# Performance work log

Hardware: AMD Instinct MI355X
Metric: run time of the kernel (lower is better)

## Reference

```python
import jax, jax.numpy as jnp
import numpy as np

N = 50000      # nodes
E = 800000     # edges (avg degree 16)
DIN = 500      # input_dim
HID = 100      # hid_dim (fixed in module)
DOUT = 64      # output_dim
EPS = 1e-5     # LayerNorm eps (torch default)


def _layer_norm(x, g, b):
    mu = jnp.mean(x, axis=-1, keepdims=True)
    var = jnp.var(x, axis=-1, keepdims=True)
    return (x - mu) / jnp.sqrt(var + EPS) * g + b


def _gcn_conv(x, src, tgt, W, b):
    # PyG GCNConv: self-loops + symmetric normalization + linear + scatter-add
    h = x @ W  # [N, out]
    idx = jnp.arange(N)
    src_sl = jnp.concatenate([src, idx])
    tgt_sl = jnp.concatenate([tgt, idx])
    deg = jax.ops.segment_sum(jnp.ones(src_sl.shape, h.dtype), tgt_sl, num_segments=N)
    dinv = jnp.where(deg > 0, deg ** -0.5, 0.0)
    norm = dinv[src_sl] * dinv[tgt_sl]  # [E+N]
    out = jax.ops.segment_sum(h[src_sl] * norm[:, None], tgt_sl, num_segments=N)
    return out + b


def setup_inputs() -> dict:
    key = jax.random.key(0)
    ks = jax.random.split(key, 10)
    glorot = lambda k, fi, fo: jax.random.normal(k, (fi, fo), jnp.float32) * np.float32(1.0 / np.sqrt(fi))
    z = lambda d: jnp.zeros((d,), jnp.float32)
    return dict(
        data_x=jax.random.normal(ks[0], (N, DIN), jnp.float32),
        data_edge_index=jax.random.randint(ks[1], (2, E), 0, N),
        data_edge_attr=jnp.zeros((E,), jnp.int32),  # single relation type
        t_W1=glorot(ks[2], DIN, HID), t_b1=z(HID), t_g1=jnp.ones((HID,), jnp.float32), t_be1=z(HID),
        t_W2=glorot(ks[3], HID, HID), t_b2=z(HID), t_g2=jnp.ones((HID,), jnp.float32), t_be2=z(HID),
        r_Wrel=glorot(ks[4], HID, HID)[None],  # [n_relations=1, H, H]
        r_Wself=glorot(ks[5], HID, HID), r_b=z(HID),
        c1_W=glorot(ks[6], HID, HID), c1_b=z(HID),
        c2_W=glorot(ks[7], HID, DOUT), c2_b=z(DOUT),
    )


def reference(data_x, data_edge_index, data_edge_attr,
              t_W1, t_b1, t_g1, t_be1, t_W2, t_b2, t_g2, t_be2,
              r_Wrel, r_Wself, r_b, c1_W, c1_b, c2_W, c2_b):
    src, tgt = data_edge_index[0], data_edge_index[1]
    # transform: Linear -> LN -> ReLU -> Linear -> LN -> ReLU
    x = jax.nn.relu(_layer_norm(data_x @ t_W1 + t_b1, t_g1, t_be1))
    x = jax.nn.relu(_layer_norm(x @ t_W2 + t_b2, t_g2, t_be2))
    # RGCN, n_relations=1, n_layers=1: per-relation message + self transform
    msgs = x[src] @ r_Wrel[0]  # edge_attr is all relation 0
    x = x @ r_Wself + jax.ops.segment_sum(msgs, tgt, num_segments=N) + r_b
    x = jax.nn.relu(x)  # dropout = identity (eval)
    x = jax.nn.relu(_gcn_conv(x, src, tgt, c1_W, c1_b))
    x = _gcn_conv(x, src, tgt, c2_W, c2_b)
    return jax.nn.log_softmax(x, axis=1)
```

## Files before the change

kernel.cpp:

```cpp
#include <hip/hip_runtime.h>
#include <hip/hip_bf16.h>

typedef __attribute__((ext_vector_type(8))) short short8;
typedef __attribute__((ext_vector_type(8))) unsigned short ushort8;
typedef __attribute__((ext_vector_type(4))) float f32x4;

static constexpr int NN = 50000;
static constexpr int NE = 800000;
static constexpr int SCAN_B = 196;

#define MFMA16x16x32 __builtin_amdgcn_mfma_f32_16x16x32_bf16

__device__ __forceinline__ float b2f(unsigned short u){
  unsigned v = ((unsigned)u) << 16;
  return __builtin_bit_cast(float, v);
}
__device__ __forceinline__ unsigned short f2b(float f){
  unsigned x = __builtin_bit_cast(unsigned, f);
  unsigned r = (x + 0x7fffu + ((x >> 16) & 1u)) >> 16;
  return (unsigned short)r;
}

__device__ __align__(256) int   g_isf32;
__device__ __align__(256) unsigned short g_W1t  [112 * 512];
__device__ __align__(256) unsigned short g_W2t  [112 * 128];
__device__ __align__(256) unsigned short g_WselfT[112 * 128];
__device__ __align__(256) unsigned short g_WrelT [112 * 128];
__device__ __align__(256) unsigned short g_c1Wt [112 * 128];
__device__ __align__(256) unsigned short g_c2Wt [64 * 128];
__device__ __align__(256) unsigned short g_bufA[(size_t)NN * 128];
__device__ __align__(256) unsigned short g_bufB[(size_t)NN * 128];
__device__ __align__(256) unsigned short g_bufC[(size_t)NN * 128];
__device__ __align__(256) int   g_deg[NN];
__device__ __align__(256) int   g_rowptr[NN + 1];
__device__ __align__(256) int   g_cursor[NN];
__device__ __align__(256) int   g_colidx[NE];
__device__ __align__(256) float g_dinv[NN];
__device__ __align__(256) int   g_partial[256];

__device__ __forceinline__ float ld_in(const void* p, int idx, int isf32){
  if (isf32) return ((const float*)p)[idx];
  return b2f(((const unsigned short*)p)[idx]);
}

__global__ void k_detect(const unsigned short* __restrict__ x){
  __shared__ int sh[256];
  int tid = threadIdx.x;
  int cnt = 0;
  for (int j = 0; j < 16; j++){
    unsigned short h = x[(size_t)(tid * 16 + j) * 2];
    int e = (h >> 7) & 0xFF;
    if (e >= 90 && e <= 160) cnt++;
  }
  sh[tid] = cnt;
  __syncthreads();
  for (int off = 128; off > 0; off >>= 1){
    if (tid < off) sh[tid] += sh[tid + off];
    __syncthreads();
  }
  if (tid == 0) g_isf32 = (sh[0] < 2458) ? 1 : 0;
}

__global__ void k_zero(){
  int i = blockIdx.x * 256 + threadIdx.x;
  if (i < NN){ g_deg[i] = 0; g_cursor[i] = 0; }
}

__device__ __forceinline__ void xp_one(const void* W, unsigned short* Wt, int idx,
                                       int K, int Nc, int Kpad, int isf32){
  int n = idx / Kpad;
  int k = idx - n * Kpad;
  float v = 0.f;
  if (n < Nc && k < K) v = ld_in(W, k * Nc + n, isf32);
  Wt[idx] = f2b(v);
}
__global__ void k_transpose_all(const void* W1, const void* W2, const void* Wself,
                                const void* Wrel, const void* c1W, const void* c2W){
  int idx = blockIdx.x * 256 + threadIdx.x;
  const int isf32 = g_isf32;
  if (idx < 57344){ xp_one(W1, g_W1t, idx, 500, 100, 512, isf32); return; }
  idx -= 57344;
  if (idx < 14336){ xp_one(W2,    g_W2t,    idx, 100, 100, 128, isf32); return; }
  idx -= 14336;
  if (idx < 14336){ xp_one(Wself, g_WselfT, idx, 100, 100, 128, isf32); return; }
  idx -= 14336;
  if (idx < 14336){ xp_one(Wrel,  g_WrelT,  idx, 100, 100, 128, isf32); return; }
  idx -= 14336;
  if (idx < 14336){ xp_one(c1W,   g_c1Wt,   idx, 100, 100, 128, isf32); return; }
  idx -= 14336;
  if (idx < 8192){  xp_one(c2W,   g_c2Wt,   idx, 100, 64,  128, isf32); }
}

__global__ void k_deg(const int* __restrict__ tgt){
  int e = blockIdx.x * 256 + threadIdx.x;
  if (e < NE) atomicAdd(&g_deg[tgt[e]], 1);
}

__global__ __launch_bounds__(256) void k_scan1(){
  __shared__ int sh[256];
  int t = threadIdx.x;
  int i = blockIdx.x * 256 + t;
  int val = (i < NN) ? g_deg[i] : 0;
  sh[t] = val;
  __syncthreads();
#pragma unroll
  for (int off = 1; off < 256; off <<= 1){
    int v = (t >= off) ? sh[t - off] : 0;
    __syncthreads();
    sh[t] += v;
    __syncthreads();
  }
  if (i < NN){
    g_rowptr[i] = sh[t] - val;
    g_dinv[i] = rsqrtf((float)(val + 1));
  }
  if (t == 255) g_partial[blockIdx.x] = sh[255];
}
__global__ __launch_bounds__(256) void k_scan2(){
  __shared__ int sh[256];
  int t = threadIdx.x;
  int val = (t < SCAN_B) ? g_partial[t] : 0;
  sh[t] = val;
  __syncthreads();
#pragma unroll
  for (int off = 1; off < 256; off <<= 1){
    int v = (t >= off) ? sh[t - off] : 0;
    __syncthreads();
    sh[t] += v;
    __syncthreads();
  }
  if (t < SCAN_B) g_partial[t] = sh[t] - val;
  if (t == 255) g_rowptr[NN] = sh[255];
}
__global__ __launch_bounds__(256) void k_scan3(){
  int i = blockIdx.x * 256 + threadIdx.x;
  if (i < NN) g_rowptr[i] += g_partial[blockIdx.x];
}

__global__ void k_fill(const int* __restrict__ src, const int* __restrict__ tgt){
  int e = blockIdx.x * 256 + threadIdx.x;
  if (e >= NE) return;
  int t = tgt[e];
  int pos = g_rowptr[t] + atomicAdd(&g_cursor[t], 1);
  g_colidx[pos] = src[e];
}

template<int MODE>
__global__ __launch_bounds__(256) void k_agg(){
  const unsigned short* x = (MODE == 1) ? g_bufC : g_bufB;
  int node = blockIdx.x * 16 + (threadIdx.x >> 4);
  if (node >= NN) return;
  const int c8 = (threadIdx.x & 15) * 8;

  float wt = (MODE != 0) ? g_dinv[node] : 1.f;
  float a[4][8];
#pragma unroll
  for (int j = 0; j < 4; j++)
#pragma unroll
    for (int k = 0; k < 8; k++) a[j][k] = 0.f;

  int p0 = g_rowptr[node], p1 = g_rowptr[node + 1];
  for (int p = p0; p < p1; p += 4){
    int   sj[4]; float wj[4];
#pragma unroll
    for (int j = 0; j < 4; j++){
      bool ok = (p + j) < p1;
      sj[j] = ok ? g_colidx[p + j] : node;
      wj[j] = ok ? ((MODE != 0) ? g_dinv[sj[j]] * wt : 1.f) : 0.f;
    }
    ushort8 r[4];
#pragma unroll
    for (int j = 0; j < 4; j++)
      r[j] = *reinterpret_cast<const ushort8*>(&x[(size_t)sj[j] * 128 + c8]);
#pragma unroll
    for (int j = 0; j < 4; j++)
#pragma unroll
      for (int k = 0; k < 8; k++) a[j][k] += wj[j] * b2f((unsigned short)r[j][k]);
  }
  if (MODE != 0){
    float ws = wt * wt;
    ushort8 sv = *reinterpret_cast<const ushort8*>(&x[(size_t)node * 128 + c8]);
#pragma unroll
    for (int k = 0; k < 8; k++) a[0][k] += ws * b2f((unsigned short)sv[k]);
  }
  ushort8 o;
#pragma unroll
  for (int k = 0; k < 8; k++)
    o[k] = f2b(a[0][k] + a[1][k] + a[2][k] + a[3][k]);
  *reinterpret_cast<ushort8*>(&g_bufA[(size_t)node * 128 + c8]) = o;
}

__global__ __launch_bounds__(256) void k_gemm1_ln(const void* __restrict__ Aext,
    const void* __restrict__ bias, const void* __restrict__ gamma,
    const void* __restrict__ beta){
  __shared__ unsigned short sA[64 * 136];
  const int tid = threadIdx.x;
  const int wave = tid >> 6, lane = tid & 63;
  const int m = lane & 15, q = lane >> 4;
  const int rowblk = blockIdx.x * 64;
  const int isf32 = g_isf32;
  const int srow = tid >> 5;
  const int scol = (tid & 31) * 4;
  f32x4 acc[7] = {};

  for (int kc = 0; kc < 4; kc++){
    __syncthreads();
#pragma unroll
    for (int ps = 0; ps < 8; ps++){
      int r = ps * 8 + srow;
      int grow = rowblk + r;
      int gcol = kc * 128 + scol;
      ushort4 vb = {0, 0, 0, 0};
      if (grow < NN && gcol + 4 <= 500){
        if (isf32){
          f32x4 v = *reinterpret_cast<const f32x4*>((const float*)Aext + (size_t)grow * 500 + gcol);
          vb.x = f2b(v[0]); vb.y = f2b(v[1]); vb.z = f2b(v[2]); vb.w = f2b(v[3]);
        } else {
          vb = *reinterpret_cast<const ushort4*>((const unsigned short*)Aext + (size_t)grow * 500 + gcol);
        }
      }
      *reinterpret_cast<ushort4*>(&sA[r * 136 + scol]) = vb;
    }
    __syncthreads();
#pragma unroll
    for (int c = 0; c < 4; c++){
      int k0 = c * 32 + q * 8;
      short8 a = *reinterpret_cast<const short8*>(&sA[(wave * 16 + m) * 136 + k0]);
      int gk0 = kc * 128 + k0;
#pragma unroll
      for (int t = 0; t < 7; t++){
        short8 b = *reinterpret_cast<const short8*>(g_W1t + (size_t)(t * 16 + m) * 512 + gk0);
        acc[t] = MFMA16x16x32(a, b, acc[t], 0, 0, 0);
      }
    }
  }

  float bf_[7], gf_[7], ef_[7];
#pragma unroll
  for (int t = 0; t < 7; t++){
    int col = t * 16 + m;
    bool ok = col < 100;
    bf_[t] = ok ? ld_in(bias, col, isf32)  : 0.f;
    gf_[t] = ok ? ld_in(gamma, col, isf32) : 0.f;
    ef_[t] = ok ? ld_in(beta, col, isf32)  : 0.f;
  }
  const int row0 = rowblk + wave * 16;
#pragma unroll
  for (int r = 0; r < 4; r++){
    float vals[7], s1 = 0.f, s2 = 0.f;
#pragma unroll
    for (int t = 0; t < 7; t++){
      int col = t * 16 + m;
      float v = (col < 100) ? (acc[t][r] + bf_[t]) : 0.f;
      vals[t] = v; s1 += v; s2 += v * v;
    }
#pragma unroll
    for (int msk = 1; msk < 16; msk <<= 1){
      s1 += __shfl_xor(s1, msk, 64);
      s2 += __shfl_xor(s2, msk, 64);
    }
    float mu = s1 * 0.01f;
    float var = fmaxf(s2 * 0.01f - mu * mu, 0.f);
    float rstd = rsqrtf(var + 1e-5f);
    int row = row0 + q * 4 + r;
    if (row < NN){
      unsigned short* orow = g_bufA + (size_t)row * 128;
#pragma unroll
      for (int t = 0; t < 7; t++){
        int col = t * 16 + m;
        float y = fmaxf((vals[t] - mu) * rstd * gf_[t] + ef_[t], 0.f);
        orow[col] = f2b((col < 100) ? y : 0.f);
      }
      orow[112 + m] = 0;
    }
  }
}

__global__ __launch_bounds__(256) void k_gemm2_ln(const void* __restrict__ bias,
    const void* __restrict__ gamma, const void* __restrict__ beta){
  const int isf32 = g_isf32;
  const int wave = threadIdx.x >> 6, lane = threadIdx.x & 63;
  const int m = lane & 15, q = lane >> 4;
  const int row0 = (blockIdx.x * 4 + wave) * 16;
  if (row0 >= NN) return;
  f32x4 acc[7] = {};
  const unsigned short* arow = g_bufA + (size_t)(row0 + m) * 128;
#pragma unroll
  for (int c = 0; c < 4; c++){
    const int k0 = c * 32 + q * 8;
    short8 a = *reinterpret_cast<const short8*>(arow + k0);
#pragma unroll
    for (int t = 0; t < 7; t++){
      short8 b = *reinterpret_cast<const short8*>(g_W2t + (size_t)(t * 16 + m) * 128 + k0);
      acc[t] = MFMA16x16x32(a, b, acc[t], 0, 0, 0);
    }
  }
  float bf_[7], gf_[7], ef_[7];
#pragma unroll
  for (int t = 0; t < 7; t++){
    int col = t * 16 + m;
    bool ok = col < 100;
    bf_[t] = ok ? ld_in(bias, col, isf32)  : 0.f;
    gf_[t] = ok ? ld_in(gamma, col, isf32) : 0.f;
    ef_[t] = ok ? ld_in(beta, col, isf32)  : 0.f;
  }
#pragma unroll
  for (int r = 0; r < 4; r++){
    float vals[7], s1 = 0.f, s2 = 0.f;
#pragma unroll
    for (int t = 0; t < 7; t++){
      int col = t * 16 + m;
      float v = (col < 100) ? (acc[t][r] + bf_[t]) : 0.f;
      vals[t] = v; s1 += v; s2 += v * v;
    }
#pragma unroll
    for (int msk = 1; msk < 16; msk <<= 1){
      s1 += __shfl_xor(s1, msk, 64);
      s2 += __shfl_xor(s2, msk, 64);
    }
    float mu = s1 * 0.01f;
    float var = fmaxf(s2 * 0.01f - mu * mu, 0.f);
    float rstd = rsqrtf(var + 1e-5f);
    unsigned short* orow = g_bufB + (size_t)(row0 + q * 4 + r) * 128;
#pragma unroll
    for (int t = 0; t < 7; t++){
      int col = t * 16 + m;
      float y = fmaxf((vals[t] - mu) * rstd * gf_[t] + ef_[t], 0.f);
      orow[col] = f2b((col < 100) ? y : 0.f);
    }
    orow[112 + m] = 0;
  }
}

template<int SEL>
__global__ __launch_bounds__(256) void k_gemm_bias_relu(const void* __restrict__ bias){
  const unsigned short* A1  = (SEL == 0) ? g_bufB : g_bufA;
  const unsigned short* B1t = (SEL == 0) ? g_WselfT : g_c1Wt;
  unsigned short* out       = (SEL == 0) ? g_bufC : g_bufB;
  const int isf32 = g_isf32;

  const int wave = threadIdx.x >> 6, lane = threadIdx.x & 63;
  const int m = lane & 15, q = lane >> 4;
  const int row0 = (blockIdx.x * 4 + wave) * 16;
  if (row0 >= NN) return;
  f32x4 acc[7] = {};
  const unsigned short* a1row = A1 + (size_t)(row0 + m) * 128;
#pragma unroll
  for (int c = 0; c < 4; c++){
    const int k0 = c * 32 + q * 8;
    short8 a = *reinterpret_cast<const short8*>(a1row + k0);
#pragma unroll
    for (int t = 0; t < 7; t++){
      short8 b = *reinterpret_cast<const short8*>(B1t + (size_t)(t * 16 + m) * 128 + k0);
      acc[t] = MFMA16x16x32(a, b, acc[t], 0, 0, 0);
    }
  }
  if (SEL == 0){
    const unsigned short* a2row = g_bufA + (size_t)(row0 + m) * 128;
#pragma unroll
    for (int c = 0; c < 4; c++){
      const int k0 = c * 32 + q * 8;
      short8 a = *reinterpret_cast<const short8*>(a2row + k0);
#pragma unroll
      for (int t = 0; t < 7; t++){
        short8 b = *reinterpret_cast<const short8*>(g_WrelT + (size_t)(t * 16 + m) * 128 + k0);
        acc[t] = MFMA16x16x32(a, b, acc[t], 0, 0, 0);
      }
    }
  }
  float bf_[7];
#pragma unroll
  for (int t = 0; t < 7; t++){
    int col = t * 16 + m;
    bf_[t] = (col < 100) ? ld_in(bias, col, isf32) : 0.f;
  }
#pragma unroll
  for (int r = 0; r < 4; r++){
    unsigned short* orow = out + (size_t)(row0 + q * 4 + r) * 128;
#pragma unroll
    for (int t = 0; t < 7; t++){
      int col = t * 16 + m;
      float y = fmaxf(acc[t][r] + bf_[t], 0.f);
      orow[col] = f2b((col < 100) ? y : 0.f);
    }
    orow[112 + m] = 0;
  }
}

__global__ __launch_bounds__(256) void k_gemm_lsm(const void* __restrict__ bias,
                                                  void* __restrict__ outv){
  const int isf32 = g_isf32;
  const int wave = threadIdx.x >> 6, lane = threadIdx.x & 63;
  const int m = lane & 15, q = lane >> 4;
  const int row0 = (blockIdx.x * 4 + wave) * 16;
  if (row0 >= NN) return;
  f32x4 acc[4] = {};
  const unsigned short* arow = g_bufA + (size_t)(row0 + m) * 128;
#pragma unroll
  for (int c = 0; c < 4; c++){
    const int k0 = c * 32 + q * 8;
    short8 a = *reinterpret_cast<const short8*>(arow + k0);
#pragma unroll
    for (int t = 0; t < 4; t++){
      short8 b = *reinterpret_cast<const short8*>(g_c2Wt + (size_t)(t * 16 + m) * 128 + k0);
      acc[t] = MFMA16x16x32(a, b, acc[t], 0, 0, 0);
    }
  }
  float bf_[4];
#pragma unroll
  for (int t = 0; t < 4; t++) bf_[t] = ld_in(bias, t * 16 + m, isf32);
#pragma unroll
  for (int r = 0; r < 4; r++){
    float vals[4], mx = -1e30f;
#pragma unroll
    for (int t = 0; t < 4; t++){
      float v = acc[t][r] + bf_[t];
      vals[t] = v; mx = fmaxf(mx, v);
    }
#pragma unroll
    for (int msk = 1; msk < 16; msk <<= 1) mx = fmaxf(mx, __shfl_xor(mx, msk, 64));
    float se = 0.f;
#pragma unroll
    for (int t = 0; t < 4; t++) se += expf(vals[t] - mx);
#pragma unroll
    for (int msk = 1; msk < 16; msk <<= 1) se += __shfl_xor(se, msk, 64);
    float lse = logf(se);
    size_t ro = (size_t)(row0 + q * 4 + r) * 64;
    if (isf32){
      float* orow = (float*)outv + ro;
#pragma unroll
      for (int t = 0; t < 4; t++) orow[t * 16 + m] = vals[t] - mx - lse;
    } else {
      unsigned short* orow = (unsigned short*)outv + ro;
#pragma unroll
      for (int t = 0; t < 4; t++) orow[t * 16 + m] = f2b(vals[t] - mx - lse);
    }
  }
}

extern "C" void kernel_launch(void* const* d_in, const int* in_sizes, int n_in,
                              void* d_out, int out_size, void* d_ws, size_t ws_size,
                              hipStream_t stream){
  (void)in_sizes; (void)n_in; (void)out_size; (void)d_ws; (void)ws_size;
  const void* data_x = d_in[0];
  const int* ei = (const int*)d_in[1];
  const int* src = ei;
  const int* tgt = ei + NE;
  const void *W1 = d_in[3], *b1 = d_in[4], *gm1 = d_in[5], *be1 = d_in[6];
  const void *W2 = d_in[7], *b2 = d_in[8], *gm2 = d_in[9], *be2 = d_in[10];
  const void *Wrel = d_in[11], *Wself = d_in[12], *rb = d_in[13];
  const void *c1W = d_in[14], *c1b = d_in[15];
  const void *c2W = d_in[16], *c2b = d_in[17];

  k_detect<<<1, 256, 0, stream>>>((const unsigned short*)data_x);
  k_zero<<<(NN + 255) / 256, 256, 0, stream>>>();
  k_transpose_all<<<(122880 + 255) / 256, 256, 0, stream>>>(W1, W2, Wself, Wrel, c1W, c2W);

  k_deg<<<(NE + 255) / 256, 256, 0, stream>>>(tgt);
  k_scan1<<<SCAN_B, 256, 0, stream>>>();
  k_scan2<<<1, 256, 0, stream>>>();
  k_scan3<<<SCAN_B, 256, 0, stream>>>();
  k_fill<<<(NE + 255) / 256, 256, 0, stream>>>(src, tgt);

  const int G64 = (NN + 63) / 64;
  const int GA  = (NN + 15) / 16;
  k_gemm1_ln<<<G64, 256, 0, stream>>>(data_x, b1, gm1, be1);
  k_gemm2_ln<<<G64, 256, 0, stream>>>(b2, gm2, be2);
  k_agg<0><<<GA, 256, 0, stream>>>();
  k_gemm_bias_relu<0><<<G64, 256, 0, stream>>>(rb);
  k_agg<1><<<GA, 256, 0, stream>>>();
  k_gemm_bias_relu<1><<<G64, 256, 0, stream>>>(c1b);
  k_agg<2><<<GA, 256, 0, stream>>>();
  k_gemm_lsm<<<G64, 256, 0, stream>>>(c2b, d_out);
}
```

Before: 526.1 us.

## Stream gemm1 A operand directly from global with register prefetch, one wave per block

The first GEMM+LayerNorm kernel stops staging the 500-wide input tile through shared memory with block-wide barriers. Each 64-thread block now handles 16 rows, and each lane loads its own row fragment straight from global memory, prefetching the next K-chunk into registers before the current MFMAs run. Out-of-range K columns are clamped to column 496; this is only correct if the padded rows of the transposed weight are zero. The change removes LDS traffic and __syncthreads stalls, at the cost of less coalesced per-instruction global access and smaller blocks.

```diff
diff --git a/kernel.cpp b/kernel.cpp
--- a/kernel.cpp
+++ b/kernel.cpp
@@ -190,48 +190,60 @@
   *reinterpret_cast<ushort8*>(&g_bufA[(size_t)node * 128 + c8]) = o;
 }
 
-__global__ __launch_bounds__(256) void k_gemm1_ln(const void* __restrict__ Aext,
+__global__ __launch_bounds__(64, 1) void k_gemm1_ln(const void* __restrict__ Aext,
     const void* __restrict__ bias, const void* __restrict__ gamma,
     const void* __restrict__ beta){
-  __shared__ unsigned short sA[64 * 136];
-  const int tid = threadIdx.x;
-  const int wave = tid >> 6, lane = tid & 63;
+  const int lane = threadIdx.x;
   const int m = lane & 15, q = lane >> 4;
-  const int rowblk = blockIdx.x * 64;
+  const int row0 = blockIdx.x * 16;
   const int isf32 = g_isf32;
-  const int srow = tid >> 5;
-  const int scol = (tid & 31) * 4;
   f32x4 acc[7] = {};
 
-  for (int kc = 0; kc < 4; kc++){
-    __syncthreads();
-#pragma unroll
-    for (int ps = 0; ps < 8; ps++){
-      int r = ps * 8 + srow;
-      int grow = rowblk + r;
-      int gcol = kc * 128 + scol;
-      ushort4 vb = {0, 0, 0, 0};
-      if (grow < NN && gcol + 4 <= 500){
-        if (isf32){
-          f32x4 v = *reinterpret_cast<const f32x4*>((const float*)Aext + (size_t)grow * 500 + gcol);
-          vb.x = f2b(v[0]); vb.y = f2b(v[1]); vb.z = f2b(v[2]); vb.w = f2b(v[3]);
-        } else {
-          vb = *reinterpret_cast<const ushort4*>((const unsigned short*)Aext + (size_t)grow * 500 + gcol);
-        }
+  if (isf32){
+    const float* arow = (const float*)Aext + (size_t)(row0 + m) * 500;
+    const int kq = q * 8;
+    f32x4 lo = *reinterpret_cast<const f32x4*>(arow + min(kq, 496));
+    f32x4 hi = *reinterpret_cast<const f32x4*>(arow + min(kq + 4, 496));
+#pragma unroll
+    for (int c = 0; c < 16; c++){
+      f32x4 lo2 = lo, hi2 = hi;
+      if (c < 15){
+        int kn = (c + 1) * 32 + kq;
+        lo2 = *reinterpret_cast<const f32x4*>(arow + min(kn, 496));
+        hi2 = *reinterpret_cast<const f32x4*>(arow + min(kn + 4, 496));
       }
-      *reinterpret_cast<ushort4*>(&sA[r * 136 + scol]) = vb;
-    }
-    __syncthreads();
-#pragma unroll
-    for (int c = 0; c < 4; c++){
-      int k0 = c * 32 + q * 8;
-      short8 a = *reinterpret_cast<const short8*>(&sA[(wave * 16 + m) * 136 + k0]);
-      int gk0 = kc * 128 + k0;
+      short8 a = {(short)f2b(lo[0]), (short)f2b(lo[1]), (short)f2b(lo[2]), (short)f2b(lo[3]),
+                  (short)f2b(hi[0]), (short)f2b(hi[1]), (short)f2b(hi[2]), (short)f2b(hi[3])};
+      const int k0 = c * 32 + kq;
 #pragma unroll
       for (int t = 0; t < 7; t++){
-        short8 b = *reinterpret_cast<const short8*>(g_W1t + (size_t)(t * 16 + m) * 512 + gk0);
+        short8 b = *reinterpret_cast<const short8*>(g_W1t + (size_t)(t * 16 + m) * 512 + k0);
         acc[t] = MFMA16x16x32(a, b, acc[t], 0, 0, 0);
       }
+      lo = lo2; hi = hi2;
+    }
+  } else {
+    const unsigned short* arow = (const unsigned short*)Aext + (size_t)(row0 + m) * 500;
+    const int kq = q * 8;
+    ushort4 lo = *reinterpret_cast<const ushort4*>(arow + min(kq, 496));
+    ushort4 hi = *reinterpret_cast<const ushort4*>(arow + min(kq + 4, 496));
+#pragma unroll
+    for (int c = 0; c < 16; c++){
+      ushort4 lo2 = lo, hi2 = hi;
+      if (c < 15){
+        int kn = (c + 1) * 32 + kq;
+        lo2 = *reinterpret_cast<const ushort4*>(arow + min(kn, 496));
+        hi2 = *reinterpret_cast<const ushort4*>(arow + min(kn + 4, 496));
+      }
+      short8 a = {(short)lo.x, (short)lo.y, (short)lo.z, (short)lo.w,
+                  (short)hi.x, (short)hi.y, (short)hi.z, (short)hi.w};
+      const int k0 = c * 32 + kq;
+#pragma unroll
+      for (int t = 0; t < 7; t++){
+        short8 b = *reinterpret_cast<const short8*>(g_W1t + (size_t)(t * 16 + m) * 512 + k0);
+        acc[t] = MFMA16x16x32(a, b, acc[t], 0, 0, 0);
+      }
+      lo = lo2; hi = hi2;
     }
   }
 
@@ -244,7 +256,6 @@
     gf_[t] = ok ? ld_in(gamma, col, isf32) : 0.f;
     ef_[t] = ok ? ld_in(beta, col, isf32)  : 0.f;
   }
-  const int row0 = rowblk + wave * 16;
 #pragma unroll
   for (int r = 0; r < 4; r++){
     float vals[7], s1 = 0.f, s2 = 0.f;
@@ -262,17 +273,14 @@
     float mu = s1 * 0.01f;
     float var = fmaxf(s2 * 0.01f - mu * mu, 0.f);
     float rstd = rsqrtf(var + 1e-5f);
-    int row = row0 + q * 4 + r;
-    if (row < NN){
-      unsigned short* orow = g_bufA + (size_t)row * 128;
-#pragma unroll
-      for (int t = 0; t < 7; t++){
-        int col = t * 16 + m;
-        float y = fmaxf((vals[t] - mu) * rstd * gf_[t] + ef_[t], 0.f);
-        orow[col] = f2b((col < 100) ? y : 0.f);
-      }
-      orow[112 + m] = 0;
-    }
+    unsigned short* orow = g_bufA + (size_t)(row0 + q * 4 + r) * 128;
+#pragma unroll
+    for (int t = 0; t < 7; t++){
+      int col = t * 16 + m;
+      float y = fmaxf((vals[t] - mu) * rstd * gf_[t] + ef_[t], 0.f);
+      orow[col] = f2b((col < 100) ? y : 0.f);
+    }
+    orow[112 + m] = 0;
   }
 }
 
@@ -464,7 +472,7 @@
 
   const int G64 = (NN + 63) / 64;
   const int GA  = (NN + 15) / 16;
-  k_gemm1_ln<<<G64, 256, 0, stream>>>(data_x, b1, gm1, be1);
+  k_gemm1_ln<<<3125, 64, 0, stream>>>(data_x, b1, gm1, be1);
   k_gemm2_ln<<<G64, 256, 0, stream>>>(b2, gm2, be2);
   k_agg<0><<<GA, 256, 0, stream>>>();
   k_gemm_bias_relu<0><<<G64, 256, 0, stream>>>(rb);
```

After: 520.8 us. About the same (-1.0%).
